# Kernel tuning notes

Hardware: AMD Instinct MI355X
Metric: run time of the kernel (lower is better)

Reference implementation:

```python
import jax, jax.numpy as jnp
import numpy as np

jax.config.update("jax_enable_x64", True)  # faithful int64 fixed-point requantize

B, K, N = 2048, 4096, 8192
INT32_MAX_MINUS = 2147418112  # threshold from multiply_by_quantize_mul


def setup_inputs() -> dict:
    key = jax.random.key(0)
    k1, k2, k3 = jax.random.split(key, 3)
    x = jax.random.randint(k1, (B, K), -128, 128, dtype=jnp.int8)
    weights = jax.random.randint(k2, (N, K), -128, 128, dtype=jnp.int8)
    bias = jax.random.randint(k3, (N, 1), -1024, 1024, dtype=jnp.int32)
    return {
        "x": x,
        "weights": weights,
        "bias": bias,
        "q_mantissa": 1431655765,   # ~2/3 in Q31 fixed point
        "exponent": -3,
        "output_zero_point": -5,
    }


def multiply_by_quantize_mul(x, q_mantissa, exponent):
    # Python precedence in original: (q_mantissa + (1<<15)) >> 16
    reduced_mantissa = ((q_mantissa + (1 << 15)) >> 16) if q_mantissa < INT32_MAX_MINUS else 32767
    total_shifts = 15 - exponent
    x = x * np.int64(reduced_mantissa)
    x = x + np.int64(1 << (total_shifts - 1))  # rounding term
    return jnp.right_shift(x, total_shifts)    # arithmetic shift on signed int64


def reference(x, weights, bias, q_mantissa, exponent, output_zero_point):
    # int8 GEMM accumulated in int32: result[b, n] = sum_k x[b, k] * w[n, k]
    acc = jnp.einsum("bk,nk->bn", x.astype(jnp.int32), weights.astype(jnp.int32))
    acc = acc + bias.T  # bias [N,1] -> [1,N], broadcast over batch
    acc = multiply_by_quantize_mul(acc.astype(jnp.int64), q_mantissa, exponent)
    acc = acc + np.int64(output_zero_point)
    out = jnp.clip(acc, -128, 127).astype(jnp.int8)
    return out
```

## Files before the change

### kernel.cpp

```cpp
#include <hip/hip_runtime.h>

#define DEVI __device__ __forceinline__

typedef int i32x4 __attribute__((ext_vector_type(4)));

static constexpr int Bdim = 2048;
static constexpr int Kdim = 4096;
static constexpr int Ndim = 8192;
static constexpr int BK   = 128;
static constexpr int NT   = Kdim / BK;

typedef __attribute__((address_space(1))) const unsigned int gas_t;
typedef __attribute__((address_space(3))) unsigned int las_t;
typedef __attribute__((address_space(3))) const char lds_cchar;

DEVI void gload_lds16(const void* g, void* l) {
    __builtin_amdgcn_global_load_lds((gas_t*)g, (las_t*)l, 16, 0, 0);
}

DEVI i32x4 dsread128(lds_cchar* p) {
    i32x4 r;
    asm volatile("ds_read_b128 %0, %1" : "=v"(r) : "v"(p));
    return r;
}

DEVI int pack4(i32x4 v) {
    return (v[0] & 255) | ((v[1] & 255) << 8) | ((v[2] & 255) << 16) | (v[3] << 24);
}

__global__ void pack_i32_to_i8(const int* __restrict__ in, char* __restrict__ out, int n16) {
    int i = blockIdx.x * blockDim.x + threadIdx.x;
    if (i >= n16) return;
    const i32x4* src = (const i32x4*)in + (size_t)i * 4;
    i32x4 r;
    r[0] = pack4(src[0]);
    r[1] = pack4(src[1]);
    r[2] = pack4(src[2]);
    r[3] = pack4(src[3]);
    ((i32x4*)out)[i] = r;
}

#define CFENCE asm volatile("" ::: "memory")
DEVI void bar() { CFENCE; __builtin_amdgcn_s_barrier(); CFENCE; }
#define WAITVM(N) asm volatile("s_waitcnt vmcnt(" #N ")" ::: "memory")
#define WAITLGKM asm volatile("s_waitcnt lgkmcnt(0)" ::: "memory")
#define SCHB __builtin_amdgcn_sched_barrier(0)
#define PRIO1 __builtin_amdgcn_s_setprio(1)
#define PRIO0 __builtin_amdgcn_s_setprio(0)

#define QUAD(MB)                                                                 \
    do {                                                                         \
        _Pragma("unroll") for (int mm = 0; mm < 4; ++mm)                         \
        _Pragma("unroll") for (int n = 0; n < 4; ++n)                            \
            acc[(MB) + mm][n] = __builtin_amdgcn_mfma_i32_16x16x64_i8(           \
                a[mm], b[n], acc[(MB) + mm][n], 0, 0, 0);                        \
    } while (0)

#define TILE(CUR, S1, S2, S3, S4, VM)                                                 \
    {                                                                                 \
        { _Pragma("unroll") for (int mm = 0; mm < 4; ++mm) a[mm] = rdA(CUR, 0, mm);   \
          _Pragma("unroll") for (int n = 0; n < 4; ++n)    b[n]  = rdB(CUR, 0, n);    \
          S1; bar(); WAITLGKM; SCHB; PRIO1; QUAD(0); PRIO0; bar(); }                  \
        { _Pragma("unroll") for (int mm = 0; mm < 4; ++mm) a[mm] = rdA(CUR, 0, 4+mm); \
          S2; bar(); WAITLGKM; SCHB; PRIO1; QUAD(4); PRIO0; bar(); }                  \
        { _Pragma("unroll") for (int mm = 0; mm < 4; ++mm) a[mm] = rdA(CUR, 1, mm);   \
          _Pragma("unroll") for (int n = 0; n < 4; ++n)    b[n]  = rdB(CUR, 1, n);    \
          S3; bar(); WAITLGKM; SCHB; PRIO1; QUAD(0); PRIO0; bar(); }                  \
        { _Pragma("unroll") for (int mm = 0; mm < 4; ++mm) a[mm] = rdA(CUR, 1, 4+mm); \
          S4; bar(); WAITLGKM; SCHB; PRIO1; QUAD(4); PRIO0; VM; bar(); }              \
    }

__global__ __launch_bounds__(512, 2)
void gemm8(const char* __restrict__ A8, const char* __restrict__ B8,
           const int* __restrict__ bias,
           const int* __restrict__ qm_p, const int* __restrict__ ex_p,
           const int* __restrict__ zp_p, int* __restrict__ out) {
    __shared__ __align__(16) char smem[131072];
    lds_cchar* sbase = (lds_cchar*)smem;

    const int tid  = threadIdx.x;
    const int wid  = tid >> 6;
    const int lane = tid & 63;
    const int l15  = lane & 15;
    const int lks  = lane >> 4;
    const int wr   = wid >> 2;
    const int wc   = wid & 3;

    const int bid = blockIdx.x;
    const int swz = (bid & 7) * 32 + (bid >> 3);
    const int bm  = swz >> 5;
    const int bn  = swz & 31;
    const int arow0 = bm * 256;
    const int brow0 = bn * 256;

    const int sw16 = (lks ^ ((l15 >> 1) & 3)) * 16;
    const int a_rd = (wr * 128 + l15) * 64 + sw16;
    const int b_rd = 65536 + (wc * 64 + l15) * 64 + sw16;

    const int st_c = (tid & 3) ^ ((tid >> 3) & 3);
    const char* agp = A8 + (size_t)(arow0 + (tid >> 2)) * Kdim + st_c * 16;
    const char* bgp = B8 + (size_t)(brow0 + (tid >> 2)) * Kdim + st_c * 16;

    auto stage = [&](int isb, int t, int ks) {
        const char* gp = (isb ? bgp : agp) + (size_t)t * BK + ks * 64;
        const int lb = (isb ? 65536 : 0) + (t & 1) * 32768 + ks * 16384 + tid * 16;
        gload_lds16(gp, &smem[lb]);
        gload_lds16(gp + (size_t)128 * Kdim, &smem[lb + 8192]);
    };
    auto rdA = [&](int buf, int ks, int m) {
        return dsread128(sbase + (buf * 32768 + ks * 16384 + a_rd + m * 1024));
    };
    auto rdB = [&](int buf, int ks, int n) {
        return dsread128(sbase + (buf * 32768 + ks * 16384 + b_rd + n * 1024));
    };

    i32x4 acc[8][4] = {};
    i32x4 a[4], b[4];

    stage(1, 0, 0); stage(0, 0, 0); stage(1, 0, 1); stage(0, 0, 1);
    stage(1, 1, 0); stage(0, 1, 0); stage(1, 1, 1);
    WAITVM(6);
    bar();

    int cur = 0;
    for (int t = 0; t < NT - 2; ++t) {
        TILE(cur,
             stage(0, t + 1, 1),
             stage(1, t + 2, 0),
             stage(0, t + 2, 0),
             stage(1, t + 2, 1),
             WAITVM(6));
        cur ^= 1;
    }
    TILE(cur,
         stage(0, NT - 1, 1),
         ((void)0), ((void)0), ((void)0),
         WAITVM(0));
    cur ^= 1;
    TILE(cur, ((void)0), ((void)0), ((void)0), ((void)0), ((void)0));

    const int qm = *qm_p;
    const int ex = *ex_p;
    const int zp = *zp_p;
    const int rm = (qm < 2147418112) ? ((qm + (1 << 15)) >> 16) : 32767;
    const int shifts = 15 - ex;
    const long long rnd = (shifts > 0) ? (1LL << (shifts - 1)) : 0;

    int bv[4];
#pragma unroll
    for (int n = 0; n < 4; ++n) bv[n] = bias[brow0 + wc * 64 + n * 16 + l15];

#pragma unroll
    for (int m = 0; m < 8; ++m) {
        const int row0 = arow0 + wr * 128 + m * 16 + lks * 4;
#pragma unroll
        for (int n = 0; n < 4; ++n) {
            const int col = brow0 + wc * 64 + n * 16 + l15;
#pragma unroll
            for (int j = 0; j < 4; ++j) {
                long long t = (long long)(acc[m][n][j] + bv[n]) * rm + rnd;
                t >>= shifts;
                t += zp;
                t = t < -128 ? -128 : (t > 127 ? 127 : t);
                out[(size_t)(row0 + j) * Ndim + col] = (int)t;
            }
        }
    }
}

extern "C" void kernel_launch(void* const* d_in, const int* in_sizes, int n_in,
                              void* d_out, int out_size, void* d_ws, size_t ws_size,
                              hipStream_t stream) {
    const int* x32  = (const int*)d_in[0];
    const int* w32  = (const int*)d_in[1];
    const int* bias = (const int*)d_in[2];
    const int* qm   = (const int*)d_in[3];
    const int* ex   = (const int*)d_in[4];
    const int* zp   = (const int*)d_in[5];
    int* out = (int*)d_out;

    char* xa = (char*)d_ws;
    char* wa = xa + (size_t)Bdim * Kdim;
    const int nx16 = Bdim * Kdim / 16;
    const int nw16 = Ndim * Kdim / 16;
    pack_i32_to_i8<<<(nx16 + 255) / 256, 256, 0, stream>>>(x32, xa, nx16);
    pack_i32_to_i8<<<(nw16 + 255) / 256, 256, 0, stream>>>(w32, wa, nw16);

    const int grid = (Bdim / 256) * (Ndim / 256);
    gemm8<<<grid, 512, 0, stream>>>(xa, wa, bias, qm, ex, zp, out);
}
```

Baseline: 105.8 us.

## Prefetch LDS fragments one phase ahead with partial lgkmcnt waits

Splits the A/B register fragments into double sets (a0/a1, b0/b1) so each phase issues the LDS reads for the next phase before running the current MFMA block. Waits become partial lgkmcnt and vmcnt counts instead of full drains, so LDS read latency can overlap the matrix math. The first phase of the next tile is read at the end of the current tile, which needs retuned vmcnt thresholds. This costs more vector registers under a 2-wave-per-SIMD launch bound, and the hand-set wait counts must be exactly right for correctness.

```diff
diff --git a/kernel.cpp b/kernel.cpp
--- a/kernel.cpp
+++ b/kernel.cpp
@@ -43,31 +43,25 @@
 #define CFENCE asm volatile("" ::: "memory")
 DEVI void bar() { CFENCE; __builtin_amdgcn_s_barrier(); CFENCE; }
 #define WAITVM(N) asm volatile("s_waitcnt vmcnt(" #N ")" ::: "memory")
-#define WAITLGKM asm volatile("s_waitcnt lgkmcnt(0)" ::: "memory")
+#define WAITLG(N) asm volatile("s_waitcnt lgkmcnt(" #N ")" ::: "memory")
 #define SCHB __builtin_amdgcn_sched_barrier(0)
 #define PRIO1 __builtin_amdgcn_s_setprio(1)
 #define PRIO0 __builtin_amdgcn_s_setprio(0)
 
-#define QUAD(MB)                                                                 \
+#define QX(MB, A, B)                                                             \
     do {                                                                         \
         _Pragma("unroll") for (int mm = 0; mm < 4; ++mm)                         \
         _Pragma("unroll") for (int n = 0; n < 4; ++n)                            \
             acc[(MB) + mm][n] = __builtin_amdgcn_mfma_i32_16x16x64_i8(           \
-                a[mm], b[n], acc[(MB) + mm][n], 0, 0, 0);                        \
+                (A)[mm], (B)[n], acc[(MB) + mm][n], 0, 0, 0);                    \
     } while (0)
 
-#define TILE(CUR, S1, S2, S3, S4, VM)                                                 \
-    {                                                                                 \
-        { _Pragma("unroll") for (int mm = 0; mm < 4; ++mm) a[mm] = rdA(CUR, 0, mm);   \
-          _Pragma("unroll") for (int n = 0; n < 4; ++n)    b[n]  = rdB(CUR, 0, n);    \
-          S1; bar(); WAITLGKM; SCHB; PRIO1; QUAD(0); PRIO0; bar(); }                  \
-        { _Pragma("unroll") for (int mm = 0; mm < 4; ++mm) a[mm] = rdA(CUR, 0, 4+mm); \
-          S2; bar(); WAITLGKM; SCHB; PRIO1; QUAD(4); PRIO0; bar(); }                  \
-        { _Pragma("unroll") for (int mm = 0; mm < 4; ++mm) a[mm] = rdA(CUR, 1, mm);   \
-          _Pragma("unroll") for (int n = 0; n < 4; ++n)    b[n]  = rdB(CUR, 1, n);    \
-          S3; bar(); WAITLGKM; SCHB; PRIO1; QUAD(0); PRIO0; bar(); }                  \
-        { _Pragma("unroll") for (int mm = 0; mm < 4; ++mm) a[mm] = rdA(CUR, 1, 4+mm); \
-          S4; bar(); WAITLGKM; SCHB; PRIO1; QUAD(4); PRIO0; VM; bar(); }              \
+#define TILE(CUR, S1, S2, S3, S4, W1, W2, RD4S, LG4)                                        \
+    {                                                                                       \
+        rdP2(CUR); S1; bar(); WAITLG(4); SCHB; PRIO1; QX(0, a0, b0); PRIO0; W1; bar();      \
+        rdP3(CUR); S2; bar(); WAITLG(8); SCHB; PRIO1; QX(4, a1, b0); PRIO0; bar();          \
+        rdP4(CUR); S3; bar(); WAITLG(4); SCHB; PRIO1; QX(0, a0, b1); PRIO0; W2; bar();      \
+        RD4S;      S4; bar(); LG4;       SCHB; PRIO1; QX(4, a1, b1); PRIO0; bar();          \
     }
 
 __global__ __launch_bounds__(512, 2)
@@ -107,20 +101,42 @@
         gload_lds16(gp, &smem[lb]);
         gload_lds16(gp + (size_t)128 * Kdim, &smem[lb + 8192]);
     };
-    auto rdA = [&](int buf, int ks, int m) {
-        return dsread128(sbase + (buf * 32768 + ks * 16384 + a_rd + m * 1024));
-    };
-    auto rdB = [&](int buf, int ks, int n) {
-        return dsread128(sbase + (buf * 32768 + ks * 16384 + b_rd + n * 1024));
-    };
 
     i32x4 acc[8][4] = {};
-    i32x4 a[4], b[4];
+    i32x4 a0[4], a1[4], b0[4], b1[4];
+
+    auto rdP1 = [&](int buf) {
+#pragma unroll
+        for (int m = 0; m < 4; ++m)
+            a0[m] = dsread128(sbase + (buf * 32768 + a_rd + m * 1024));
+#pragma unroll
+        for (int n = 0; n < 4; ++n)
+            b0[n] = dsread128(sbase + (buf * 32768 + b_rd + n * 1024));
+    };
+    auto rdP2 = [&](int buf) {
+#pragma unroll
+        for (int m = 0; m < 4; ++m)
+            a1[m] = dsread128(sbase + (buf * 32768 + a_rd + (4 + m) * 1024));
+    };
+    auto rdP3 = [&](int buf) {
+#pragma unroll
+        for (int m = 0; m < 4; ++m)
+            a0[m] = dsread128(sbase + (buf * 32768 + 16384 + a_rd + m * 1024));
+#pragma unroll
+        for (int n = 0; n < 4; ++n)
+            b1[n] = dsread128(sbase + (buf * 32768 + 16384 + b_rd + n * 1024));
+    };
+    auto rdP4 = [&](int buf) {
+#pragma unroll
+        for (int m = 0; m < 4; ++m)
+            a1[m] = dsread128(sbase + (buf * 32768 + 16384 + a_rd + (4 + m) * 1024));
+    };
 
     stage(1, 0, 0); stage(0, 0, 0); stage(1, 0, 1); stage(0, 0, 1);
     stage(1, 1, 0); stage(0, 1, 0); stage(1, 1, 1);
-    WAITVM(6);
+    WAITVM(10);
     bar();
+    rdP1(0);
 
     int cur = 0;
     for (int t = 0; t < NT - 2; ++t) {
@@ -129,15 +145,20 @@
              stage(1, t + 2, 0),
              stage(0, t + 2, 0),
              stage(1, t + 2, 1),
-             WAITVM(6));
+             WAITVM(8), WAITVM(8),
+             rdP1(cur ^ 1), WAITLG(8));
         cur ^= 1;
     }
     TILE(cur,
          stage(0, NT - 1, 1),
          ((void)0), ((void)0), ((void)0),
-         WAITVM(0));
+         WAITVM(8), WAITVM(4),
+         rdP1(cur ^ 1), WAITLG(8));
     cur ^= 1;
-    TILE(cur, ((void)0), ((void)0), ((void)0), ((void)0), ((void)0));
+    TILE(cur,
+         ((void)0), ((void)0), ((void)0), ((void)0),
+         WAITVM(0), ((void)0),
+         ((void)0), WAITLG(0));
 
     const int qm = *qm_p;
     const int ex = *ex_p;
```

Measured after the change: 107.2 us. About the same (+1.4%).

## Load B operands directly from global into registers, halve LDS footprint

Applied to the files above, without the earlier changes.

B tiles are no longer staged through LDS. Each wave now loads its B fragments straight into registers with global_load_dwordx4, double-buffered across k-halves. Only A stays in LDS, so shared memory drops from 128KB to 64KB, which could allow more occupancy or less LDS traffic. In exchange, each wave issues redundant uncoalesced-ish global loads for B (the four waves sharing a column block each fetch it), and the vmcnt waits now have to cover both the register loads and the LDS-staged loads.

```diff
diff --git a/kernel.cpp b/kernel.cpp
--- a/kernel.cpp
+++ b/kernel.cpp
@@ -21,6 +21,12 @@
 DEVI i32x4 dsread128(lds_cchar* p) {
     i32x4 r;
     asm volatile("ds_read_b128 %0, %1" : "=v"(r) : "v"(p));
+    return r;
+}
+
+DEVI i32x4 gload128(const char* p) {
+    i32x4 r;
+    asm volatile("global_load_dwordx4 %0, %1, off" : "=v"(r) : "v"(p));
     return r;
 }
 
@@ -43,31 +49,29 @@
 #define CFENCE asm volatile("" ::: "memory")
 DEVI void bar() { CFENCE; __builtin_amdgcn_s_barrier(); CFENCE; }
 #define WAITVM(N) asm volatile("s_waitcnt vmcnt(" #N ")" ::: "memory")
-#define WAITLGKM asm volatile("s_waitcnt lgkmcnt(0)" ::: "memory")
+#define WAITLG0 asm volatile("s_waitcnt lgkmcnt(0)" ::: "memory")
 #define SCHB __builtin_amdgcn_sched_barrier(0)
 #define PRIO1 __builtin_amdgcn_s_setprio(1)
 #define PRIO0 __builtin_amdgcn_s_setprio(0)
 
-#define QUAD(MB)                                                                 \
+#define QX(MB, BREG)                                                             \
     do {                                                                         \
         _Pragma("unroll") for (int mm = 0; mm < 4; ++mm)                         \
         _Pragma("unroll") for (int n = 0; n < 4; ++n)                            \
             acc[(MB) + mm][n] = __builtin_amdgcn_mfma_i32_16x16x64_i8(           \
-                a[mm], b[n], acc[(MB) + mm][n], 0, 0, 0);                        \
+                a[mm], (BREG)[n], acc[(MB) + mm][n], 0, 0, 0);                   \
     } while (0)
 
-#define TILE(CUR, S1, S2, S3, S4, VM)                                                 \
-    {                                                                                 \
-        { _Pragma("unroll") for (int mm = 0; mm < 4; ++mm) a[mm] = rdA(CUR, 0, mm);   \
-          _Pragma("unroll") for (int n = 0; n < 4; ++n)    b[n]  = rdB(CUR, 0, n);    \
-          S1; bar(); WAITLGKM; SCHB; PRIO1; QUAD(0); PRIO0; bar(); }                  \
-        { _Pragma("unroll") for (int mm = 0; mm < 4; ++mm) a[mm] = rdA(CUR, 0, 4+mm); \
-          S2; bar(); WAITLGKM; SCHB; PRIO1; QUAD(4); PRIO0; bar(); }                  \
-        { _Pragma("unroll") for (int mm = 0; mm < 4; ++mm) a[mm] = rdA(CUR, 1, mm);   \
-          _Pragma("unroll") for (int n = 0; n < 4; ++n)    b[n]  = rdB(CUR, 1, n);    \
-          S3; bar(); WAITLGKM; SCHB; PRIO1; QUAD(0); PRIO0; bar(); }                  \
-        { _Pragma("unroll") for (int mm = 0; mm < 4; ++mm) a[mm] = rdA(CUR, 1, 4+mm); \
-          S4; bar(); WAITLGKM; SCHB; PRIO1; QUAD(4); PRIO0; VM; bar(); }              \
+#define TILE(CUR, W1, IB1, IA1, W2, IB0, IA0)                                       \
+    {                                                                               \
+        rdA(CUR, 0, 0); W1; IB1; IA1; bar(); WAITLG0; SCHB;                         \
+        PRIO1; QX(0, b0); PRIO0; bar();                                             \
+        rdA(CUR, 0, 4); bar(); WAITLG0; SCHB;                                       \
+        PRIO1; QX(4, b0); PRIO0; bar();                                             \
+        rdA(CUR, 1, 0); W2; IB0; IA0; bar(); WAITLG0; SCHB;                         \
+        PRIO1; QX(0, b1); PRIO0; bar();                                             \
+        rdA(CUR, 1, 4); bar(); WAITLG0; SCHB;                                       \
+        PRIO1; QX(4, b1); PRIO0; bar();                                             \
     }
 
 __global__ __launch_bounds__(512, 2)
@@ -75,7 +79,7 @@
            const int* __restrict__ bias,
            const int* __restrict__ qm_p, const int* __restrict__ ex_p,
            const int* __restrict__ zp_p, int* __restrict__ out) {
-    __shared__ __align__(16) char smem[131072];
+    __shared__ __align__(16) char smem[65536];
     lds_cchar* sbase = (lds_cchar*)smem;
 
     const int tid  = threadIdx.x;
@@ -94,50 +98,56 @@
     const int brow0 = bn * 256;
 
     const int sw16 = (lks ^ ((l15 >> 1) & 3)) * 16;
-    const int a_rd = (wr * 128 + l15) * 64 + sw16;
-    const int b_rd = 65536 + (wc * 64 + l15) * 64 + sw16;
+    const int a_rd0 = (wr * 128 + l15) * 64 + sw16;
 
     const int st_c = (tid & 3) ^ ((tid >> 3) & 3);
     const char* agp = A8 + (size_t)(arow0 + (tid >> 2)) * Kdim + st_c * 16;
-    const char* bgp = B8 + (size_t)(brow0 + (tid >> 2)) * Kdim + st_c * 16;
-
-    auto stage = [&](int isb, int t, int ks) {
-        const char* gp = (isb ? bgp : agp) + (size_t)t * BK + ks * 64;
-        const int lb = (isb ? 65536 : 0) + (t & 1) * 32768 + ks * 16384 + tid * 16;
+
+    auto stage = [&](int t, int ks) {
+        const char* gp = agp + (size_t)t * BK + ks * 64;
+        const int lb = (t & 1) * 32768 + ks * 16384 + tid * 16;
         gload_lds16(gp, &smem[lb]);
         gload_lds16(gp + (size_t)128 * Kdim, &smem[lb + 8192]);
     };
-    auto rdA = [&](int buf, int ks, int m) {
-        return dsread128(sbase + (buf * 32768 + ks * 16384 + a_rd + m * 1024));
+
+    const char* bb[4];
+#pragma unroll
+    for (int n = 0; n < 4; ++n)
+        bb[n] = B8 + (size_t)(brow0 + wc * 64 + n * 16 + l15) * Kdim + lks * 16;
+
+    i32x4 acc[8][4] = {};
+    i32x4 a[4], b0[4], b1[4];
+
+    auto rdAimpl = [&](int buf, int ks, int h) {
+#pragma unroll
+        for (int m = 0; m < 4; ++m)
+            a[m] = dsread128(sbase + (buf * 32768 + ks * 16384 + a_rd0 + (h + m) * 1024));
     };
-    auto rdB = [&](int buf, int ks, int n) {
-        return dsread128(sbase + (buf * 32768 + ks * 16384 + b_rd + n * 1024));
+#define rdA(BUF, KS, H) rdAimpl(BUF, KS, H)
+
+    auto loadB = [&](i32x4* dst, int t, int kk) {
+#pragma unroll
+        for (int n = 0; n < 4; ++n)
+            dst[n] = gload128(bb[n] + (size_t)t * BK + kk * 64);
     };
 
-    i32x4 acc[8][4] = {};
-    i32x4 a[4], b[4];
-
-    stage(1, 0, 0); stage(0, 0, 0); stage(1, 0, 1); stage(0, 0, 1);
-    stage(1, 1, 0); stage(0, 1, 0); stage(1, 1, 1);
-    WAITVM(6);
+    stage(0, 0); stage(0, 1); stage(1, 0);
+    loadB(b0, 0, 0);
+    WAITVM(0);
     bar();
 
-    int cur = 0;
     for (int t = 0; t < NT - 2; ++t) {
+        const int cur = t & 1;
         TILE(cur,
-             stage(0, t + 1, 1),
-             stage(1, t + 2, 0),
-             stage(0, t + 2, 0),
-             stage(1, t + 2, 1),
-             WAITVM(6));
-        cur ^= 1;
+             WAITVM(2), loadB(b1, t, 1), stage(t + 1, 1),
+             WAITVM(2), loadB(b0, t + 1, 0), stage(t + 2, 0));
     }
-    TILE(cur,
-         stage(0, NT - 1, 1),
-         ((void)0), ((void)0), ((void)0),
-         WAITVM(0));
-    cur ^= 1;
-    TILE(cur, ((void)0), ((void)0), ((void)0), ((void)0), ((void)0));
+    TILE((NT - 2) & 1,
+         WAITVM(2), loadB(b1, NT - 2, 1), stage(NT - 1, 1),
+         WAITVM(2), loadB(b0, NT - 1, 0), ((void)0));
+    TILE((NT - 1) & 1,
+         WAITVM(0), loadB(b1, NT - 1, 1), ((void)0),
+         WAITVM(0), ((void)0), ((void)0));
 
     const int qm = *qm_p;
     const int ex = *ex_p;
```

Measured after the change: 132.1 us. +24.9%, slower.
